# Kernel optimization log

Hardware: AMD Instinct MI355X
Metric: run time of the kernel (lower is better)

Reference implementation:

```python
import jax, jax.numpy as jnp
import numpy as np


def setup_inputs() -> dict:
    key = jax.random.key(0)
    k1, k2 = jax.random.split(key)
    B, Lq, Lk, D = 8, 2048, 2048, 1024
    output = jax.random.normal(k1, (B, Lq, D), dtype=jnp.float32)
    inputs = jax.random.normal(k2, (B, Lk, D), dtype=jnp.float32)
    return {"output": output, "inputs": inputs}


def reference(output, inputs):
    # scores: (B, Lq, Lk) = output @ inputs^T  (no scaling, no mask — matches torch.bmm)
    scores = jnp.einsum("bqd,bkd->bqk", output, inputs)
    attn = jax.nn.softmax(scores, axis=-1)
    # context: (B, Lq, D) = attn @ inputs
    context = jnp.einsum("bqk,bkd->bqd", attn, inputs)
    return (context, attn)
```

## Files before the change

kernel.cpp:

```cpp
#include <hip/hip_runtime.h>

#define LQ 2048
#define LK 2048
#define DD 1024
#define NB 8
#define NSL 8192
#define SSHIFT 125.0f

typedef __attribute__((ext_vector_type(4))) float f4;
typedef __attribute__((ext_vector_type(4))) float f32x4;
typedef __attribute__((ext_vector_type(8))) short s16x8;
typedef __attribute__((ext_vector_type(8))) _Float16 h16x8;
typedef __attribute__((ext_vector_type(4))) _Float16 h16x4;
typedef __attribute__((ext_vector_type(2))) unsigned long long u64x2_t;

__device__ __forceinline__ void gload_lds16(const _Float16* g, const _Float16* l) {
  __builtin_amdgcn_global_load_lds((const __attribute__((address_space(1))) void*)g,
                                   (__attribute__((address_space(3))) void*)l, 16, 0, 0);
}


__global__ __launch_bounds__(256) void conv_all(const float* __restrict__ Q,
                                                const float* __restrict__ K,
                                                _Float16* __restrict__ Qh,
                                                _Float16* __restrict__ Kh,
                                                _Float16* __restrict__ KT) {
  __shared__ _Float16 tile[64][66];
  const int b = blockIdx.z;
  const int t = threadIdx.x, tr = t >> 4, tc = t & 15;
  if (blockIdx.x >= 32) {
    const int r0 = (blockIdx.x - 32) * 64, d0 = blockIdx.y * 64;
    const float* Qb = Q + ((size_t)b * LQ + r0) * DD + d0;
    _Float16* Qo = Qh + ((size_t)b * LQ + r0) * DD + d0;
#pragma unroll
    for (int i = 0; i < 4; ++i) {
      int rr = tr + i * 16;
      f4 v = *(const f4*)(Qb + (size_t)rr * DD + tc * 4);
      h16x4 h;
#pragma unroll
      for (int j = 0; j < 4; ++j) h[j] = (_Float16)v[j];
      *(h16x4*)(Qo + (size_t)rr * DD + tc * 4) = h;
    }
  } else {
    const int k0 = blockIdx.x * 64, d0 = blockIdx.y * 64;
#pragma unroll
    for (int i = 0; i < 4; ++i) {
      int kk = tr + i * 16;
      f4 v = *(const f4*)(K + ((size_t)b * LK + k0 + kk) * DD + d0 + tc * 4);
      h16x4 h;
#pragma unroll
      for (int j = 0; j < 4; ++j) { h[j] = (_Float16)v[j]; tile[tc * 4 + j][kk] = h[j]; }
      *(h16x4*)(Kh + ((size_t)b * LK + k0 + kk) * DD + d0 + tc * 4) = h;
    }
    __syncthreads();
#pragma unroll
    for (int i = 0; i < 4; ++i) {
      int dd = tr + i * 16;
      h16x4 o;
#pragma unroll
      for (int j = 0; j < 4; ++j) o[j] = tile[dd][tc * 4 + j];
      *(h16x4*)(KT + ((size_t)b * DD + d0 + dd) * LK + k0 + tc * 4) = o;
    }
  }
}


__device__ __forceinline__ void load_af(const _Float16* ASm, int p, int mh,
                                        int wm, int lm, int grp, h16x8 af[4][2]) {
#pragma unroll
  for (int mti = 0; mti < 4; ++mti) {
    int slot = wm * 64 + mti * 16 + lm;
    const _Float16* base = ASm + (p * 2 + mh) * NSL + slot * 64;
#pragma unroll
    for (int kb = 0; kb < 2; ++kb) {
      int uu = (kb * 4 + grp) ^ (slot & 7);
      af[mti][kb] = *(const h16x8*)(base + uu * 8);
    }
  }
}

__device__ __forceinline__ void load_bf(const _Float16* BSm, int p, int nh,
                                        int wn, int lm, int grp, h16x8 bf[2][2]) {
#pragma unroll
  for (int nti = 0; nti < 2; ++nti) {
    int slot = wn * 32 + nti * 16 + lm;
    const _Float16* base = BSm + (p * 2 + nh) * NSL + slot * 64;
#pragma unroll
    for (int kb = 0; kb < 2; ++kb) {
      int uu = (kb * 4 + grp) ^ (slot & 7);
      bf[nti][kb] = *(const h16x8*)(base + uu * 8);
    }
  }
}

__device__ __forceinline__ void mfma_quad(f32x4 acc[8][4], const h16x8 af[4][2],
                                          const h16x8 bf[2][2], int mh, int nh) {
  __builtin_amdgcn_s_setprio(1);
#pragma unroll
  for (int nti = 0; nti < 2; ++nti)
#pragma unroll
    for (int mti = 0; mti < 4; ++mti)
#pragma unroll
      for (int kb = 0; kb < 2; ++kb)
        acc[mh * 4 + mti][nh * 2 + nti] = __builtin_amdgcn_mfma_f32_16x16x32_f16(
            af[mti][kb], bf[nti][kb], acc[mh * 4 + mti][nh * 2 + nti], 0, 0, 0);
  __builtin_amdgcn_s_setprio(0);
}

__device__ __forceinline__ void phase_mid() {
  __builtin_amdgcn_s_barrier();
  __builtin_amdgcn_sched_barrier(0);
}
__device__ __forceinline__ void phase_end() { __builtin_amdgcn_s_barrier(); }
__device__ __forceinline__ void phase_end_v() {
  asm volatile("s_waitcnt vmcnt(6)" ::: "memory");
  __builtin_amdgcn_s_barrier();
}

template <typename OutT>
__device__ __forceinline__ void gemm8_body(
    const _Float16* __restrict__ A, const _Float16* __restrict__ B, OutT* __restrict__ C,
    int Klen, int lda, int ldb, int kmask, int ldc, long sA, long sB, long sC,
    float cshift, _Float16* smem) {
  _Float16* ASm = smem;
  _Float16* BSm = smem + 4 * NSL;

  const int nwgx = gridDim.x, nwgy = gridDim.y;
  const int nwg = nwgx * nwgy * gridDim.z;
  const int lin = blockIdx.x + nwgx * (blockIdx.y + nwgy * blockIdx.z);
  const int swzid = (lin & 7) * (nwg >> 3) + (lin >> 3);
  const int bx = swzid % nwgx;
  const int rest = swzid / nwgx;
  const int by = rest % nwgy, bz = rest / nwgy;

  const _Float16* Ab = A + (size_t)bz * sA;
  const _Float16* Bb = B + (size_t)bz * sB;
  OutT* Cb = C + (size_t)bz * sC;
  const int m0 = by * 256, n0 = bx * 256;

  const int tid = threadIdx.x, lane = tid & 63, w = tid >> 6;
  const int wm = w >> 2, wn = w & 3;
  const int lm = lane & 15, grp = lane >> 4;

  const _Float16* pAj[2];
  const _Float16* pBj[2];
#pragma unroll
  for (int j = 0; j < 2; ++j) {
    int s = (j * 8 + w) * 8 + (lane >> 3);
    int colp = ((lane & 7) ^ (s & 7)) * 8;
    int rA = (s & 63) | ((s >> 6) << 7);
    int rB = (s & 31) | ((s >> 5) << 6);
    pAj[j] = Ab + (size_t)(m0 + rA) * lda + colp;
    pBj[j] = Bb + (size_t)(n0 + rB) * ldb + colp;
  }
  const size_t hA = (size_t)64 * lda;
  const size_t hB = (size_t)32 * ldb;

#define STAGE_A(p, h, kk) do { \
    gload_lds16(pAj[0] + ((h) ? hA : 0) + (kk), ASm + ((p) * 2 + (h)) * NSL + w * 512); \
    gload_lds16(pAj[1] + ((h) ? hA : 0) + (kk), ASm + ((p) * 2 + (h)) * NSL + 4096 + w * 512); \
  } while (0)
#define STAGE_B(p, h, kk) do { \
    gload_lds16(pBj[0] + ((h) ? hB : 0) + (kk), BSm + ((p) * 2 + (h)) * NSL + w * 512); \
    gload_lds16(pBj[1] + ((h) ? hB : 0) + (kk), BSm + ((p) * 2 + (h)) * NSL + 4096 + w * 512); \
  } while (0)

  f32x4 acc[8][4] = {};
  const int NT = Klen / 64;

  STAGE_A(0, 0, 0);
  STAGE_B(0, 1, 0);
  STAGE_A(0, 1, 0);
  STAGE_B(0, 0, 0);
  STAGE_A(1, 0, 64);
  STAGE_B(1, 1, 64 & kmask);
  STAGE_A(1, 1, 64);
  asm volatile("s_waitcnt vmcnt(6)" ::: "memory");
  __builtin_amdgcn_s_barrier();

  h16x8 af[4][2], bf0[2][2], bf1[2][2];

  for (int it = 0; it < NT / 2; ++it) {
    const int t = 2 * it;
    const int p = t & 1, q = p ^ 1;
    const int kt1 = (t + 1) * 64;
    const int kt2 = ((t + 2 < NT) ? (t + 2) : (NT - 1)) * 64;
    const int kt3 = ((t + 3 < NT) ? (t + 3) : (NT - 1)) * 64;
    const int kt1b = kt1 & kmask, kt2b = kt2 & kmask, kt3b = kt3 & kmask;

    load_af(ASm, p, 0, wm, lm, grp, af);
    load_bf(BSm, p, 0, wn, lm, grp, bf0);
    STAGE_B(q, 0, kt1b);
    phase_mid(); mfma_quad(acc, af, bf0, 0, 0); phase_end();
    load_bf(BSm, p, 1, wn, lm, grp, bf1);
    STAGE_A(p, 0, kt2);
    phase_mid(); mfma_quad(acc, af, bf1, 0, 1); phase_end();
    load_af(ASm, p, 1, wm, lm, grp, af);
    STAGE_B(p, 1, kt2b);
    phase_mid(); mfma_quad(acc, af, bf1, 1, 1); phase_end();
    STAGE_A(p, 1, kt2);
    phase_mid(); mfma_quad(acc, af, bf0, 1, 0); phase_end_v();
    load_af(ASm, q, 0, wm, lm, grp, af);
    load_bf(BSm, q, 0, wn, lm, grp, bf0);
    STAGE_B(p, 0, kt2b);
    phase_mid(); mfma_quad(acc, af, bf0, 0, 0); phase_end();
    load_bf(BSm, q, 1, wn, lm, grp, bf1);
    STAGE_A(q, 0, kt3);
    phase_mid(); mfma_quad(acc, af, bf1, 0, 1); phase_end();
    load_af(ASm, q, 1, wm, lm, grp, af);
    STAGE_B(q, 1, kt3b);
    phase_mid(); mfma_quad(acc, af, bf1, 1, 1); phase_end();
    STAGE_A(q, 1, kt3);
    phase_mid(); mfma_quad(acc, af, bf0, 1, 0); phase_end_v();
  }

#pragma unroll
  for (int mh = 0; mh < 2; ++mh)
#pragma unroll
    for (int mti = 0; mti < 4; ++mti) {
      int row0 = m0 + wm * 128 + mh * 64 + mti * 16 + grp * 4;
#pragma unroll
      for (int nh = 0; nh < 2; ++nh)
#pragma unroll
        for (int nti = 0; nti < 2; ++nti) {
          int col = n0 + wn * 64 + nh * 32 + nti * 16 + lm;
#pragma unroll
          for (int qq = 0; qq < 4; ++qq)
            Cb[(size_t)(row0 + qq) * ldc + col] =
                (OutT)(acc[mh * 4 + mti][nh * 2 + nti][qq] + cshift);
        }
    }
#undef STAGE_A
#undef STAGE_B
}

__global__ __launch_bounds__(512, 2) void gemm8_f32(
    const _Float16* __restrict__ A, const _Float16* __restrict__ B, float* __restrict__ C,
    int Klen, int lda, int ldb, int kmask, int ldc, long sA, long sB, long sC) {
  extern __shared__ _Float16 smem[];
  gemm8_body<float>(A, B, C, Klen, lda, ldb, kmask, ldc, sA, sB, sC, 0.0f, smem);
}

__global__ __launch_bounds__(512, 2) void gemm8_f16(
    const _Float16* __restrict__ A, const _Float16* __restrict__ B, _Float16* __restrict__ C,
    int Klen, int lda, int ldb, int kmask, int ldc, long sA, long sB, long sC) {
  extern __shared__ _Float16 smem[];
  gemm8_body<_Float16>(A, B, C, Klen, lda, ldb, kmask, ldc, sA, sB, sC, -SSHIFT, smem);
}


__global__ __launch_bounds__(256) void softmax_f16(_Float16* __restrict__ SP,
                                                   float* __restrict__ A) {
  __shared__ float red[4];
  const int row = blockIdx.x;
  _Float16* pr = SP + (size_t)row * LK;
  const int t = threadIdx.x, lane = t & 63, w = t >> 6;
  h16x8 v = *(const h16x8*)(pr + t * 8);
  float x[8];
#pragma unroll
  for (int i = 0; i < 8; ++i) x[i] = (float)v[i];

  float m = x[0];
#pragma unroll
  for (int i = 1; i < 8; ++i) m = fmaxf(m, x[i]);
#pragma unroll
  for (int off = 32; off > 0; off >>= 1) m = fmaxf(m, __shfl_xor(m, off));
  if (lane == 0) red[w] = m;
  __syncthreads();
  m = fmaxf(fmaxf(red[0], red[1]), fmaxf(red[2], red[3]));
  __syncthreads();

  float e[8];
  float s = 0.f;
#pragma unroll
  for (int i = 0; i < 8; ++i) { e[i] = __expf(x[i] - m); s += e[i]; }
#pragma unroll
  for (int off = 32; off > 0; off >>= 1) s += __shfl_xor(s, off);
  if (lane == 0) red[w] = s;
  __syncthreads();
  s = red[0] + red[1] + red[2] + red[3];
  const float inv = 1.0f / s;

  f4 a0, a1;
  h16x8 o;
#pragma unroll
  for (int i = 0; i < 8; ++i) {
    float y = e[i] * inv;
    if (i < 4) a0[i] = y; else a1[i - 4] = y;
    o[i] = (_Float16)y;
  }
  float* ar = A + (size_t)row * LK + t * 8;
  *(f4*)ar = a0;
  *(f4*)(ar + 4) = a1;
  *(h16x8*)(pr + t * 8) = o;
}


__global__ __launch_bounds__(256) void softmax_rows(float* __restrict__ S,
                                                    _Float16* __restrict__ P) {
  __shared__ float red[4];
  const int row = blockIdx.x;
  float* p = S + (size_t)row * LK;
  const int t = threadIdx.x;
  const int lane = t & 63, w = t >> 6;
  f4* p4 = (f4*)p;
  f4 v0 = p4[t], v1 = p4[t + 256];

  float m = fmaxf(fmaxf(fmaxf(v0[0], v0[1]), fmaxf(v0[2], v0[3])),
                  fmaxf(fmaxf(v1[0], v1[1]), fmaxf(v1[2], v1[3])));
#pragma unroll
  for (int off = 32; off > 0; off >>= 1) m = fmaxf(m, __shfl_xor(m, off));
  if (lane == 0) red[w] = m;
  __syncthreads();
  m = fmaxf(fmaxf(red[0], red[1]), fmaxf(red[2], red[3]));
  __syncthreads();

  f4 e0, e1;
  float s = 0.f;
#pragma unroll
  for (int i = 0; i < 4; ++i) { e0[i] = __expf(v0[i] - m); s += e0[i]; }
#pragma unroll
  for (int i = 0; i < 4; ++i) { e1[i] = __expf(v1[i] - m); s += e1[i]; }
#pragma unroll
  for (int off = 32; off > 0; off >>= 1) s += __shfl_xor(s, off);
  if (lane == 0) red[w] = s;
  __syncthreads();
  s = red[0] + red[1] + red[2] + red[3];
  float inv = 1.0f / s;
  e0 *= inv; e1 *= inv;
  p4[t] = e0; p4[t + 256] = e1;
  if (P) {
    h16x4 a, bb;
#pragma unroll
    for (int i = 0; i < 4; ++i) { a[i] = (_Float16)e0[i]; bb[i] = (_Float16)e1[i]; }
    _Float16* pr = P + (size_t)row * LK;
    *(h16x4*)(pr + t * 4) = a;
    *(h16x4*)(pr + 1024 + t * 4) = bb;
  }
}


__device__ __forceinline__ unsigned int f2bf_bits(float x) {
  unsigned int u = __float_as_uint(x);
  return (u + 0x7fffu + ((u >> 16) & 1u)) >> 16;
}
__device__ __forceinline__ float bf2f(unsigned int h) { return __uint_as_float(h << 16); }
__device__ __forceinline__ void hilo4(const f4 v, unsigned long long& ph, unsigned long long& pl) {
  unsigned int h[4], l[4];
#pragma unroll
  for (int i = 0; i < 4; ++i) {
    h[i] = f2bf_bits(v[i]);
    float rr = v[i] - bf2f(h[i]);
    l[i] = f2bf_bits(rr);
  }
  ph = (unsigned long long)h[0] | ((unsigned long long)h[1] << 16) |
       ((unsigned long long)h[2] << 32) | ((unsigned long long)h[3] << 48);
  pl = (unsigned long long)l[0] | ((unsigned long long)l[1] << 16) |
       ((unsigned long long)l[2] << 32) | ((unsigned long long)l[3] << 48);
}
__device__ __forceinline__ unsigned long long pack4bf(float a, float b, float c, float d) {
  return (unsigned long long)f2bf_bits(a) | ((unsigned long long)f2bf_bits(b) << 16) |
         ((unsigned long long)f2bf_bits(c) << 32) | ((unsigned long long)f2bf_bits(d) << 48);
}
__device__ __forceinline__ s16x8 mkfrag(unsigned long long u0, unsigned long long u1) {
  u64x2_t t; t[0] = u0; t[1] = u1;
  return __builtin_bit_cast(s16x8, t);
}
__device__ __forceinline__ f32x4 mfma16b(s16x8 a, s16x8 b, f32x4 c) {
  return __builtin_amdgcn_mfma_f32_16x16x32_bf16(a, b, c, 0, 0, 0);
}

__global__ __launch_bounds__(256) void gemm1_scores(
    const float* __restrict__ Q, const float* __restrict__ K, float* __restrict__ S) {
  __shared__ unsigned long long Ah[128 * 8], Al[128 * 8], Bh[128 * 8], Bl[128 * 8];
  const int b = blockIdx.z;
  const float* Qb = Q + (size_t)b * LQ * DD;
  const float* Kb = K + (size_t)b * LK * DD;
  float* Sb = S + (size_t)b * LQ * LK;
  const int m0 = blockIdx.y * 128, n0 = blockIdx.x * 128;
  const int t = threadIdx.x;
  const int lane = t & 63, w = t >> 6;
  const int wr = (w >> 1) * 64, wc = (w & 1) * 64;
  const int lm = lane & 15, grp = lane >> 4;
  f32x4 acc[4][4] = {};
  const int r = t >> 1, hf = t & 1;
  const int sw_st = ((r >> 1) ^ (r >> 4)) & 7;
  const f4* srcA = (const f4*)(Qb + (size_t)(m0 + r) * DD) + hf * 4;
  const f4* srcB = (const f4*)(Kb + (size_t)(n0 + r) * DD) + hf * 4;
  for (int k0 = 0; k0 < DD; k0 += 32) {
#pragma unroll
    for (int u = 0; u < 4; ++u) {
      f4 v = srcA[u];
      unsigned long long ph, pl;
      hilo4(v, ph, pl);
      int idx = r * 8 + ((hf * 4 + u) ^ sw_st);
      Ah[idx] = ph; Al[idx] = pl;
    }
#pragma unroll
    for (int u = 0; u < 4; ++u) {
      f4 v = srcB[u];
      unsigned long long ph, pl;
      hilo4(v, ph, pl);
      int idx = r * 8 + ((hf * 4 + u) ^ sw_st);
      Bh[idx] = ph; Bl[idx] = pl;
    }
    srcA += 8; srcB += 8;
    __syncthreads();
    s16x8 afh[4], afl[4];
#pragma unroll
    for (int mt = 0; mt < 4; ++mt) {
      int row = wr + mt * 16 + lm;
      int sw = ((row >> 1) ^ (row >> 4)) & 7;
      int ua = (2 * grp) ^ sw;
      int base = row * 8;
      afh[mt] = mkfrag(Ah[base + ua], Ah[base + (ua ^ 1)]);
      afl[mt] = mkfrag(Al[base + ua], Al[base + (ua ^ 1)]);
    }
#pragma unroll
    for (int nt = 0; nt < 4; ++nt) {
      int row = wc + nt * 16 + lm;
      int sw = ((row >> 1) ^ (row >> 4)) & 7;
      int ua = (2 * grp) ^ sw;
      int base = row * 8;
      s16x8 bfh = mkfrag(Bh[base + ua], Bh[base + (ua ^ 1)]);
      s16x8 bfl = mkfrag(Bl[base + ua], Bl[base + (ua ^ 1)]);
#pragma unroll
      for (int mt = 0; mt < 4; ++mt) {
        acc[mt][nt] = mfma16b(afh[mt], bfh, acc[mt][nt]);
        acc[mt][nt] = mfma16b(afh[mt], bfl, acc[mt][nt]);
        acc[mt][nt] = mfma16b(afl[mt], bfh, acc[mt][nt]);
      }
    }
    __syncthreads();
  }
#pragma unroll
  for (int mt = 0; mt < 4; ++mt) {
    int rowb = m0 + wr + mt * 16 + grp * 4;
#pragma unroll
    for (int nt = 0; nt < 4; ++nt) {
      int col = n0 + wc + nt * 16 + lm;
#pragma unroll
      for (int q = 0; q < 4; ++q)
        Sb[(size_t)(rowb + q) * LK + col] = acc[mt][nt][q];
    }
  }
}

__global__ __launch_bounds__(256) void gemm2_ctx(
    const float* __restrict__ P, const float* __restrict__ K, float* __restrict__ C) {
  __shared__ unsigned long long As[128 * 8], Bs[128 * 8];
  const int b = blockIdx.z;
  const float* Pb = P + (size_t)b * LQ * LK;
  const float* Kb = K + (size_t)b * LK * DD;
  float* Cb = C + (size_t)b * LQ * DD;
  const int m0 = blockIdx.y * 128, n0 = blockIdx.x * 128;
  const int t = threadIdx.x, lane = t & 63, w = t >> 6;
  const int wr = (w >> 1) * 64, wc = (w & 1) * 64;
  const int lm = lane & 15, grp = lane >> 4;
  f32x4 acc[4][4] = {};
  const int r = t >> 1, hf = t & 1;
  const int sw_a = ((r >> 1) ^ (r >> 4)) & 7;
  const f4* srcA = (const f4*)(Pb + (size_t)(m0 + r) * LK) + hf * 4;
  const int ka = t >> 5, bi = t & 31;
  const float* srcB0 = Kb + (size_t)(4 * ka) * DD + n0 + 4 * bi;
  for (int k0 = 0; k0 < LK; k0 += 32) {
#pragma unroll
    for (int u = 0; u < 4; ++u) {
      f4 v = srcA[u];
      As[r * 8 + ((hf * 4 + u) ^ sw_a)] = pack4bf(v[0], v[1], v[2], v[3]);
    }
    srcA += 8;
    const float* sB = srcB0 + (size_t)k0 * DD;
    f4 rv[4];
#pragma unroll
    for (int rr = 0; rr < 4; ++rr) rv[rr] = *(const f4*)(sB + (size_t)rr * DD);
#pragma unroll
    for (int q = 0; q < 4; ++q) {
      int n = 4 * bi + q;
      int sw = ((n >> 1) ^ (n >> 4)) & 7;
      Bs[n * 8 + (ka ^ sw)] = pack4bf(rv[0][q], rv[1][q], rv[2][q], rv[3][q]);
    }
    __syncthreads();
    s16x8 af2[4];
#pragma unroll
    for (int mt = 0; mt < 4; ++mt) {
      int row = wr + mt * 16 + lm;
      int sw = ((row >> 1) ^ (row >> 4)) & 7;
      int ua = (2 * grp) ^ sw;
      af2[mt] = mkfrag(As[row * 8 + ua], As[row * 8 + (ua ^ 1)]);
    }
#pragma unroll
    for (int nt = 0; nt < 4; ++nt) {
      int row = wc + nt * 16 + lm;
      int sw = ((row >> 1) ^ (row >> 4)) & 7;
      int ua = (2 * grp) ^ sw;
      s16x8 bf = mkfrag(Bs[row * 8 + ua], Bs[row * 8 + (ua ^ 1)]);
#pragma unroll
      for (int mt = 0; mt < 4; ++mt)
        acc[mt][nt] = mfma16b(af2[mt], bf, acc[mt][nt]);
    }
    __syncthreads();
  }
#pragma unroll
  for (int mt = 0; mt < 4; ++mt) {
    int rowb = m0 + wr + mt * 16 + grp * 4;
#pragma unroll
    for (int nt = 0; nt < 4; ++nt) {
      int col = n0 + wc + nt * 16 + lm;
#pragma unroll
      for (int q = 0; q < 4; ++q)
        Cb[(size_t)(rowb + q) * DD + col] = acc[mt][nt][q];
    }
  }
}


extern "C" void kernel_launch(void* const* d_in, const int* in_sizes, int n_in,
                              void* d_out, int out_size, void* d_ws, size_t ws_size,
                              hipStream_t stream) {
  const float* Q = (const float*)d_in[0];
  const float* K = (const float*)d_in[1];
  float* ctx  = (float*)d_out;
  float* attn = (float*)d_out + (size_t)NB * LQ * DD;

  const size_t nQh = (size_t)NB * LQ * DD;
  const size_t nKh = (size_t)NB * LK * DD;
  const size_t nKT = (size_t)NB * DD * LK;
  const size_t nPw = (size_t)NB * LQ * LK;
  const size_t need = (nQh + nKh + nKT + nPw) * sizeof(_Float16);

  if (ws_size >= need) {
    _Float16* Qh = (_Float16*)d_ws;
    _Float16* Kh = Qh + nQh;
    _Float16* KT = Kh + nKh;
    _Float16* Pw = KT + nKT;

    (void)hipFuncSetAttribute((const void*)gemm8_f16,
                              hipFuncAttributeMaxDynamicSharedMemorySize, 131072);
    (void)hipFuncSetAttribute((const void*)gemm8_f32,
                              hipFuncAttributeMaxDynamicSharedMemorySize, 131072);

    conv_all<<<dim3(64, 16, NB), 256, 0, stream>>>(Q, K, Qh, Kh, KT);

    gemm8_f16<<<dim3(LK / 256, LQ / 256, NB), 512, 131072, stream>>>(
        Qh, Kh, Pw, 1024, 1024, 1024, 1023, LK,
        (long)LQ * DD, (long)LK * DD, (long)LQ * LK);

    softmax_f16<<<dim3(NB * LQ), 256, 0, stream>>>(Pw, attn);

    gemm8_f32<<<dim3(DD / 256, LQ / 256, NB), 512, 131072, stream>>>(
        Pw, KT, ctx, 2048, 2048, 2048, 2047, DD,
        (long)LQ * LK, (long)DD * LK, (long)LQ * DD);
  } else {
    gemm1_scores<<<dim3(LK / 128, LQ / 128, NB), 256, 0, stream>>>(Q, K, attn);
    softmax_rows<<<dim3(NB * LQ), 256, 0, stream>>>(attn, nullptr);
    gemm2_ctx<<<dim3(DD / 128, LQ / 128, NB), 256, 0, stream>>>(attn, K, ctx);
  }
}
```

Measured before the change: 228.3 us.

## Restructure GEMM main loop into two-phase-per-tile schedule with fewer barriers

Measured after the change: 224.1 us, median of 2. No clear change (-1.8%).

```diff
diff --git a/kernel.cpp b/kernel.cpp
--- a/kernel.cpp
+++ b/kernel.cpp
@@ -93,8 +93,9 @@
   }
 }
 
-__device__ __forceinline__ void mfma_quad(f32x4 acc[8][4], const h16x8 af[4][2],
-                                          const h16x8 bf[2][2], int mh, int nh) {
+__device__ __forceinline__ void mfma_pair(f32x4 acc[8][4], const h16x8 af[4][2],
+                                          const h16x8 bf0[2][2], const h16x8 bf1[2][2],
+                                          int mh) {
   __builtin_amdgcn_s_setprio(1);
 #pragma unroll
   for (int nti = 0; nti < 2; ++nti)
@@ -102,18 +103,27 @@
     for (int mti = 0; mti < 4; ++mti)
 #pragma unroll
       for (int kb = 0; kb < 2; ++kb)
-        acc[mh * 4 + mti][nh * 2 + nti] = __builtin_amdgcn_mfma_f32_16x16x32_f16(
-            af[mti][kb], bf[nti][kb], acc[mh * 4 + mti][nh * 2 + nti], 0, 0, 0);
+        acc[mh * 4 + mti][nti] = __builtin_amdgcn_mfma_f32_16x16x32_f16(
+            af[mti][kb], bf0[nti][kb], acc[mh * 4 + mti][nti], 0, 0, 0);
+#pragma unroll
+  for (int nti = 0; nti < 2; ++nti)
+#pragma unroll
+    for (int mti = 0; mti < 4; ++mti)
+#pragma unroll
+      for (int kb = 0; kb < 2; ++kb)
+        acc[mh * 4 + mti][2 + nti] = __builtin_amdgcn_mfma_f32_16x16x32_f16(
+            af[mti][kb], bf1[nti][kb], acc[mh * 4 + mti][2 + nti], 0, 0, 0);
   __builtin_amdgcn_s_setprio(0);
 }
 
-__device__ __forceinline__ void phase_mid() {
+__device__ __forceinline__ void pre_mfma() { __builtin_amdgcn_sched_barrier(0); }
+__device__ __forceinline__ void phase_end() { __builtin_amdgcn_s_barrier(); }
+__device__ __forceinline__ void phase_end_v6() {
+  asm volatile("s_waitcnt vmcnt(6)" ::: "memory");
   __builtin_amdgcn_s_barrier();
-  __builtin_amdgcn_sched_barrier(0);
-}
-__device__ __forceinline__ void phase_end() { __builtin_amdgcn_s_barrier(); }
-__device__ __forceinline__ void phase_end_v() {
-  asm volatile("s_waitcnt vmcnt(6)" ::: "memory");
+}
+__device__ __forceinline__ void phase_end_v4() {
+  asm volatile("s_waitcnt vmcnt(4)" ::: "memory");
   __builtin_amdgcn_s_barrier();
 }
 
@@ -174,44 +184,43 @@
   STAGE_B(0, 0, 0);
   STAGE_A(1, 0, 64);
   STAGE_B(1, 1, 64 & kmask);
-  STAGE_A(1, 1, 64);
-  asm volatile("s_waitcnt vmcnt(6)" ::: "memory");
+  asm volatile("s_waitcnt vmcnt(4)" ::: "memory");
   __builtin_amdgcn_s_barrier();
 
   h16x8 af[4][2], bf0[2][2], bf1[2][2];
 
   for (int it = 0; it < NT / 2; ++it) {
     const int t = 2 * it;
-    const int p = t & 1, q = p ^ 1;
     const int kt1 = (t + 1) * 64;
     const int kt2 = ((t + 2 < NT) ? (t + 2) : (NT - 1)) * 64;
     const int kt3 = ((t + 3 < NT) ? (t + 3) : (NT - 1)) * 64;
     const int kt1b = kt1 & kmask, kt2b = kt2 & kmask, kt3b = kt3 & kmask;
 
-    load_af(ASm, p, 0, wm, lm, grp, af);
-    load_bf(BSm, p, 0, wn, lm, grp, bf0);
-    STAGE_B(q, 0, kt1b);
-    phase_mid(); mfma_quad(acc, af, bf0, 0, 0); phase_end();
-    load_bf(BSm, p, 1, wn, lm, grp, bf1);
-    STAGE_A(p, 0, kt2);
-    phase_mid(); mfma_quad(acc, af, bf1, 0, 1); phase_end();
-    load_af(ASm, p, 1, wm, lm, grp, af);
-    STAGE_B(p, 1, kt2b);
-    phase_mid(); mfma_quad(acc, af, bf1, 1, 1); phase_end();
-    STAGE_A(p, 1, kt2);
-    phase_mid(); mfma_quad(acc, af, bf0, 1, 0); phase_end_v();
-    load_af(ASm, q, 0, wm, lm, grp, af);
-    load_bf(BSm, q, 0, wn, lm, grp, bf0);
-    STAGE_B(p, 0, kt2b);
-    phase_mid(); mfma_quad(acc, af, bf0, 0, 0); phase_end();
-    load_bf(BSm, q, 1, wn, lm, grp, bf1);
-    STAGE_A(q, 0, kt3);
-    phase_mid(); mfma_quad(acc, af, bf1, 0, 1); phase_end();
-    load_af(ASm, q, 1, wm, lm, grp, af);
-    STAGE_B(q, 1, kt3b);
-    phase_mid(); mfma_quad(acc, af, bf1, 1, 1); phase_end();
-    STAGE_A(q, 1, kt3);
-    phase_mid(); mfma_quad(acc, af, bf0, 1, 0); phase_end_v();
+    load_af(ASm, 0, 0, wm, lm, grp, af);
+    load_bf(BSm, 0, 0, wn, lm, grp, bf0);
+    load_bf(BSm, 0, 1, wn, lm, grp, bf1);
+    STAGE_B(1, 0, kt1b);
+    STAGE_A(1, 1, kt1);
+    pre_mfma(); mfma_pair(acc, af, bf0, bf1, 0); phase_end();
+
+    load_af(ASm, 0, 1, wm, lm, grp, af);
+    STAGE_A(0, 0, kt2);
+    STAGE_B(0, 1, kt2b);
+    STAGE_B(0, 0, kt2b);
+    pre_mfma(); mfma_pair(acc, af, bf0, bf1, 1);
+    phase_end_v6();
+
+    load_af(ASm, 1, 0, wm, lm, grp, af);
+    load_bf(BSm, 1, 0, wn, lm, grp, bf0);
+    load_bf(BSm, 1, 1, wn, lm, grp, bf1);
+    STAGE_A(0, 1, kt2);
+    pre_mfma(); mfma_pair(acc, af, bf0, bf1, 0); phase_end();
+
+    load_af(ASm, 1, 1, wm, lm, grp, af);
+    STAGE_A(1, 0, kt3);
+    STAGE_B(1, 1, kt3b);
+    pre_mfma(); mfma_pair(acc, af, bf0, bf1, 1);
+    phase_end_v4();
   }
 
 #pragma unroll
```
